# Kernel optimization log

Hardware: AMD Instinct MI355X
Metric: run time of the kernel (lower is better)

The kernel has to match this reference:

```python
import jax, jax.numpy as jnp
import numpy as np

B, N, D = 1024, 7, 1024
SQRT_D = float(np.sqrt(D))
MAX_CTX, MAX_VIB = 0.24, 0.26
VIB_IDX, CTX_IDX = 3, N - 1

ADJ = jnp.asarray(np.array([
    [1, 1, 0, 0, 1, 1, 1],
    [1, 1, 1, 1, 1, 1, 1],
    [0, 1, 1, 0, 1, 0, 1],
    [0, 1, 0, 1, 1, 1, 1],
    [1, 1, 1, 1, 1, 1, 1],
    [1, 1, 0, 1, 1, 1, 1],
    [1, 1, 1, 1, 1, 1, 1]], dtype=np.float32))


def _gelu(x):
    return jax.nn.gelu(x, approximate=False)


def setup_inputs() -> dict:
    key = jax.random.key(0)
    ks = jax.random.split(key, 20)
    s = 0.02
    def w(k, shape):
        return jax.random.normal(k, shape, dtype=jnp.float32) * s
    return {
        "nodes": jax.random.normal(ks[0], (B, N, D), dtype=jnp.float32),
        "Wq": w(ks[1], (D, D)), "bq": jnp.zeros((D,), jnp.float32),
        "Wk": w(ks[2], (D, D)), "bk": jnp.zeros((D,), jnp.float32),
        "Wv": w(ks[3], (D, D)), "bv": jnp.zeros((D,), jnp.float32),
        "We1": w(ks[4], (3 * D, D)), "be1": jnp.zeros((D,), jnp.float32),
        "We2": w(ks[5], (D, 1)), "be2": jnp.zeros((1,), jnp.float32),
        "Wu1": w(ks[6], (2 * D, D)), "bu1": jnp.zeros((D,), jnp.float32),
        "Wu2": w(ks[7], (D, D)), "bu2": jnp.zeros((D,), jnp.float32),
        "Wi1": w(ks[8], (2 * D, D)), "bi1": jnp.zeros((D,), jnp.float32),
        "Wi2": w(ks[9], (D, 1)), "bi2": jnp.zeros((1,), jnp.float32),
    }


def _cap_importance(imp):
    cap = jnp.ones((N,), imp.dtype).at[VIB_IDX].set(MAX_VIB).at[CTX_IDX].set(MAX_CTX)
    free = jnp.ones((N,), imp.dtype).at[VIB_IDX].set(0.0).at[CTX_IDX].set(0.0)[None, :]
    capped = jnp.minimum(imp, cap[None, :])
    free_mass = (imp * free).sum(axis=1, keepdims=True)
    residual = jnp.clip(1.0 - capped.sum(axis=1, keepdims=True), 0.0)
    uniform = free / jnp.maximum(free.sum(axis=1, keepdims=True), 1.0)
    free_share = jnp.where(free_mass > 1e-6,
                           imp * free / jnp.maximum(free_mass, 1e-6),
                           uniform)
    redis = capped + free_share * residual
    return redis / jnp.maximum(redis.sum(axis=1, keepdims=True), 1e-6)


def _physics_loss(upd):
    norms = jnp.linalg.norm(upd, axis=-1)  # [B,N]
    dots = jnp.einsum('bnd,bmd->bnm', upd, upd)
    cos = dots / jnp.maximum(norms[:, :, None] * norms[:, None, :], 1e-8)
    eye = jnp.eye(N, dtype=upd.dtype)
    edge_loss = ((1.0 - cos) * ADJ[None]).sum() / jnp.maximum(ADJ.sum() * upd.shape[0], 1.0) * upd.shape[0]
    # note: torch sums over batch too -> divide by ADJ.sum() only
    edge_loss = ((1.0 - cos) * ADJ[None]).sum() / jnp.maximum(ADJ.sum(), 1.0)
    non_mask = (1.0 - ADJ) * (1.0 - eye)
    non_loss = (jax.nn.relu(cos - 0.35) * non_mask[None]).sum() / jnp.maximum(non_mask.sum(), 1.0)
    return edge_loss + 0.5 * non_loss


def _alignment_loss(upd, fused):
    fn = fused / jnp.maximum(jnp.linalg.norm(fused, axis=-1, keepdims=True), 1e-12)
    nn_ = upd / jnp.maximum(jnp.linalg.norm(upd, axis=-1, keepdims=True), 1e-12)
    cos = jnp.einsum('bnd,bd->bn', nn_, fn)
    return (1.0 - cos).mean()


def reference(nodes, Wq, bq, Wk, bk, Wv, bv, We1, be1, We2, be2,
              Wu1, bu1, Wu2, bu2, Wi1, bi1, Wi2, bi2):
    q = nodes @ Wq + bq
    k = nodes @ Wk + bk
    v = nodes @ Wv + bv
    logits = jnp.einsum('bnd,bmd->bnm', q, k) / SQRT_D
    # edge gate: cat([left, right, ctx]) @ We1 == left@Wa + right@Wb + ctx@Wc
    Wa, Wb, Wc = We1[:D], We1[D:2 * D], We1[2 * D:]
    la = nodes @ Wa                      # [B,N,D] (left varies over axis n)
    rb = nodes @ Wb                      # [B,N,D] (right varies over axis m)
    cc = nodes[:, -1] @ Wc               # [B,D]   (ctx broadcast)
    h = la[:, :, None, :] + rb[:, None, :, :] + cc[:, None, None, :] + be1
    edge_logits = (_gelu(h) @ We2 + be2)[..., 0]  # [B,N,N]
    masked = logits + edge_logits + (ADJ[None] - 1.0) * 10000.0
    attn = jax.nn.softmax(masked, axis=-1)
    messages = jnp.einsum('bnm,bmd->bnd', attn, v)
    upd_in = jnp.concatenate([nodes, messages], axis=-1)
    updated = _gelu(upd_in @ Wu1 + bu1) @ Wu2 + bu2 + nodes
    gq = jnp.broadcast_to(updated[:, -1:, :], updated.shape)
    imp_in = jnp.concatenate([updated, gq], axis=-1)
    imp_logits = (_gelu(imp_in @ Wi1 + bi1) @ Wi2 + bi2)[..., 0]
    imp = jax.nn.softmax(imp_logits, axis=-1)
    imp = _cap_importance(imp)
    fused = jnp.einsum('bn,bnd->bd', imp, updated)
    phys = _physics_loss(updated)
    align = _alignment_loss(updated, fused)
    return (fused, updated, imp, attn, phys + align * 0.0, align)
```

## Files before the change

kernel.cpp:

```cpp
#include <hip/hip_runtime.h>
#include <hip/hip_bf16.h>


typedef __attribute__((ext_vector_type(8))) short bf16x8;
typedef __attribute__((ext_vector_type(4))) float f32x4;

__constant__ float c_adj[49] = {
    1,1,0,0,1,1,1,
    1,1,1,1,1,1,1,
    0,1,1,0,1,0,1,
    0,1,0,1,1,1,1,
    1,1,1,1,1,1,1,
    1,1,0,1,1,1,1,
    1,1,1,1,1,1,1};

__device__ __forceinline__ float gelu_f(float x) {
    float z = fabsf(x) * 0.70710678118654752f;
    float t = 1.0f / (1.0f + 0.3275911f * z);
    float poly = ((((1.061405429f * t - 1.453152027f) * t + 1.421413741f) * t
                  - 0.284496736f) * t + 0.254829592f) * t;
    float e = __expf(-z * z);
    float erf_abs = 1.0f - poly * e;
    float erf = copysignf(erf_abs, x);
    return 0.5f * x * (1.0f + erf);
}
__device__ __forceinline__ float b2f(unsigned short u) {
    unsigned int x = ((unsigned int)u) << 16;
    union { unsigned int i; float f; } c; c.i = x; return c.f;
}
__device__ __forceinline__ unsigned short f2b(float f) {
    __hip_bfloat16 h = __float2bfloat16(f);
    union { __hip_bfloat16 b; unsigned short u; } c; c.b = h; return c.u;
}

__device__ __forceinline__ void gload_lds16(const void* g, void* l) {
    __builtin_amdgcn_global_load_lds(
        (const __attribute__((address_space(1))) unsigned int*)g,
        (__attribute__((address_space(3))) unsigned int*)l, 16, 0, 0);
}

__device__ __forceinline__ int maprow(int r, int mode) {
    if (mode == 1) return r * 7 + 6;
    if (mode == 2) return r - r % 7 + 6;
    return r;
}

__global__ __launch_bounds__(512, 4) void gemm128x8w(
    const unsigned short* __restrict__ A1, int a1Mode,
    const unsigned short* __restrict__ A2, int a2Mode,
    const unsigned short* __restrict__ WT, int ldw,
    const float* __restrict__ bias,
    const float* __restrict__ resid,
    float* __restrict__ Cf,
    unsigned short* __restrict__ Cb, size_t segStride,
    int K, int act)
{
    __shared__ short As[3][128 * 32];
    __shared__ short Bs[3][128 * 32];
    const int tid = threadIdx.x;
    const int lane = tid & 63;
    const int w = tid >> 6;
    const int wr = (w >> 2) * 64;
    const int wc = (w & 3) * 32;

    int lin = blockIdx.y * gridDim.x + blockIdx.x;
    const int nwg = gridDim.x * gridDim.y;
    const int cpx = nwg >> 3;
    lin = (lin & 7) * cpx + (lin >> 3);
    const int row0 = (lin / gridDim.x) * 128;
    const int col0 = (lin % gridDim.x) * 128;

    const int fr = lane & 15;
    const int fko = (((lane >> 4) ^ ((fr >> 1) & 3)) << 3);

    const int sm_ = tid >> 2, sch = tid & 3;
    const int skc = (sch ^ ((sm_ >> 1) & 3)) * 8;
    const int ldsoff = tid * 8;

    const int NTt = K >> 5;

    auto stage = [&](int ktn) {
        int k0n = ktn * 32;
        const unsigned short* srcA; int mode; int kbase;
        if (k0n < 1024) { srcA = A1; mode = a1Mode; kbase = k0n; }
        else            { srcA = A2; mode = a2Mode; kbase = k0n - 1024; }
        int slot = ktn % 3;
        int rr = maprow(row0 + sm_, mode);
        gload_lds16(srcA + (size_t)rr * 1024 + kbase + skc, &As[slot][ldsoff]);
        gload_lds16(WT + (size_t)(col0 + sm_) * ldw + k0n + skc, &Bs[slot][ldsoff]);
    };

    f32x4 acc[4][2] = {};

    stage(0);
    if (NTt > 1) stage(1);
    asm volatile("s_waitcnt vmcnt(2)" ::: "memory");
    asm volatile("s_barrier" ::: "memory");

    for (int kt = 0; kt < NTt; ++kt) {
        const short* Ab = &As[kt % 3][0];
        const short* Bb = &Bs[kt % 3][0];

        if (kt + 2 < NTt) stage(kt + 2);

        bf16x8 af[4], bfv[2];
        #pragma unroll
        for (int i = 0; i < 4; ++i)
            af[i] = *(const bf16x8*)(Ab + (wr + i * 16 + fr) * 32 + fko);
        #pragma unroll
        for (int j = 0; j < 2; ++j)
            bfv[j] = *(const bf16x8*)(Bb + (wc + j * 16 + fr) * 32 + fko);

        __builtin_amdgcn_s_setprio(1);
        #pragma unroll
        for (int i = 0; i < 4; ++i)
            #pragma unroll
            for (int j = 0; j < 2; ++j)
                acc[i][j] = __builtin_amdgcn_mfma_f32_16x16x32_bf16(
                    af[i], bfv[j], acc[i][j], 0, 0, 0);
        __builtin_amdgcn_s_setprio(0);

        if (kt < NTt - 2) asm volatile("s_waitcnt vmcnt(2)" ::: "memory");
        else              asm volatile("s_waitcnt vmcnt(0)" ::: "memory");
        asm volatile("s_barrier" ::: "memory");
    }

    const int qrow = (lane >> 4) * 4;
    const int qcol = lane & 15;
    #pragma unroll
    for (int i = 0; i < 4; ++i) {
        int rbase = row0 + wr + i * 16 + qrow;
        #pragma unroll
        for (int j = 0; j < 2; ++j) {
            int c = col0 + wc + j * 16 + qcol;
            float bv = bias ? bias[c] : 0.0f;
            int seg = c >> 10, c0 = c & 1023;
            #pragma unroll
            for (int reg = 0; reg < 4; ++reg) {
                int r = rbase + reg;
                float vv = acc[i][j][reg] + bv;
                if (act) vv = gelu_f(vv);
                if (resid) vv += resid[(size_t)r * 1024 + c];
                if (Cf) Cf[(size_t)r * 1024 + c] = vv;
                if (Cb) Cb[(size_t)seg * segStride + (size_t)r * 1024 + c0] = f2b(vv);
            }
        }
    }
}

__global__ __launch_bounds__(256) void gemm64x128(
    const unsigned short* __restrict__ A1, int a1Mode,
    const unsigned short* __restrict__ A2, int a2Mode,
    const unsigned short* __restrict__ WT, int ldw,
    const float* __restrict__ bias,
    const float* __restrict__ resid,
    float* __restrict__ Cf,
    unsigned short* __restrict__ Cb,
    int K, int act)
{
    __shared__ short As[64 * 32];
    __shared__ short Bs[128 * 32];
    const int tid = threadIdx.x;
    const int lane = tid & 63;
    const int w = tid >> 6;
    const int wc = w * 32;
    const int row0 = blockIdx.y * 64;
    const int col0 = blockIdx.x * 128;
    const int fr = lane & 15;
    const int fko = (((lane >> 4) ^ ((fr >> 1) & 3)) << 3);

    f32x4 acc[4][2] = {};

    for (int k0 = 0; k0 < K; k0 += 32) {
        const unsigned short* srcA; int mode; int kbase;
        if (k0 < 1024) { srcA = A1; mode = a1Mode; kbase = k0; }
        else           { srcA = A2; mode = a2Mode; kbase = k0 - 1024; }
        {
            int m = tid >> 2, ch = tid & 3;
            int kc = (ch ^ ((m >> 1) & 3)) * 8;
            int rr = maprow(row0 + m, mode);
            gload_lds16(srcA + (size_t)rr * 1024 + kbase + kc, &As[tid * 8]);
        }
        #pragma unroll
        for (int rnd = 0; rnd < 2; ++rnd) {
            int c = rnd * 256 + tid;
            int n = c >> 2, ch = c & 3;
            int kc = (ch ^ ((n >> 1) & 3)) * 8;
            gload_lds16(WT + (size_t)(col0 + n) * ldw + k0 + kc, &Bs[c * 8]);
        }
        __syncthreads();
        bf16x8 af[4], bf_[2];
        #pragma unroll
        for (int i = 0; i < 4; ++i)
            af[i] = *(const bf16x8*)(&As[(i * 16 + fr) * 32 + fko]);
        #pragma unroll
        for (int j = 0; j < 2; ++j)
            bf_[j] = *(const bf16x8*)(&Bs[(wc + j * 16 + fr) * 32 + fko]);
        #pragma unroll
        for (int i = 0; i < 4; ++i)
            #pragma unroll
            for (int j = 0; j < 2; ++j)
                acc[i][j] = __builtin_amdgcn_mfma_f32_16x16x32_bf16(
                    af[i], bf_[j], acc[i][j], 0, 0, 0);
        __syncthreads();
    }

    const int qrow = (lane >> 4) * 4;
    const int qcol = lane & 15;
    #pragma unroll
    for (int i = 0; i < 4; ++i) {
        int rbase = row0 + i * 16 + qrow;
        #pragma unroll
        for (int j = 0; j < 2; ++j) {
            int c = col0 + wc + j * 16 + qcol;
            float bv = bias ? bias[c] : 0.0f;
            #pragma unroll
            for (int reg = 0; reg < 4; ++reg) {
                int r = rbase + reg;
                float vv = acc[i][j][reg] + bv;
                if (act) vv = gelu_f(vv);
                if (resid) vv += resid[(size_t)r * 1024 + c];
                if (Cf) Cf[(size_t)r * 1024 + c] = vv;
                if (Cb) Cb[(size_t)r * 1024 + c] = f2b(vv);
            }
        }
    }
}

__global__ __launch_bounds__(256) void cast_f2b(
    const float* __restrict__ in, unsigned short* __restrict__ out, int n)
{
    int i = (blockIdx.x * 256 + threadIdx.x) * 4;
    if (i >= n) return;
    float4 v = *(const float4*)(in + i);
    ushort4 o;
    o.x = f2b(v.x); o.y = f2b(v.y); o.z = f2b(v.z); o.w = f2b(v.w);
    *(ushort4*)(out + i) = o;
}

__global__ __launch_bounds__(256) void tcast_all(
    const float* __restrict__ Wq, const float* __restrict__ Wk,
    const float* __restrict__ Wv, const float* __restrict__ We1,
    const float* __restrict__ Wu1, const float* __restrict__ Wu2,
    const float* __restrict__ Wi1,
    unsigned short* __restrict__ WT_all, unsigned short* __restrict__ Wu1T,
    unsigned short* __restrict__ Wu2T, unsigned short* __restrict__ Wi1T)
{
    const int z = blockIdx.z;
    const float* src; unsigned short* dst; int R;
    switch (z) {
        case 0: src = Wq;            dst = WT_all;               R = 1024; break;
        case 1: src = Wk;            dst = WT_all + 1024 * 1024; R = 1024; break;
        case 2: src = Wv;            dst = WT_all + 2048 * 1024; R = 1024; break;
        case 3: src = We1;           dst = WT_all + 3072 * 1024; R = 1024; break;
        case 4: src = We1 + 1048576; dst = WT_all + 4096 * 1024; R = 1024; break;
        case 5: src = We1 + 2097152; dst = WT_all + 5120 * 1024; R = 1024; break;
        case 6: src = Wu1;           dst = Wu1T;                 R = 2048; break;
        case 7: src = Wu2;           dst = Wu2T;                 R = 1024; break;
        default: src = Wi1;          dst = Wi1T;                 R = 2048; break;
    }
    const int rt = blockIdx.y * 32;
    if (rt >= R) return;
    const int ct = blockIdx.x * 32;
    __shared__ float t[32][33];
    const int tx = threadIdx.x & 31, ty = threadIdx.x >> 5;
    #pragma unroll
    for (int s = 0; s < 4; ++s)
        t[ty + s * 8][tx] = src[(size_t)(rt + ty + s * 8) * 1024 + ct + tx];
    __syncthreads();
    #pragma unroll
    for (int s = 0; s < 4; ++s)
        dst[(size_t)(ct + ty + s * 8) * R + rt + tx] = f2b(t[tx][ty + s * 8]);
}

__global__ void build_bias(const float* __restrict__ bq,
                           const float* __restrict__ bk,
                           const float* __restrict__ bv,
                           float* __restrict__ bias_all,
                           float* __restrict__ acc)
{
    int i = blockIdx.x * 256 + threadIdx.x;
    if (i < 4) acc[i] = 0.f;
    if (i >= 5120) return;
    int seg = i >> 10, c = i & 1023;
    float v = 0.f;
    if (seg == 0) v = bq[c];
    else if (seg == 1) v = bk[c];
    else if (seg == 2) v = bv[c];
    bias_all[i] = v;
}

__global__ __launch_bounds__(256) void attn_msg_b(
    const unsigned short* __restrict__ q, const unsigned short* __restrict__ k,
    const unsigned short* __restrict__ v,
    const unsigned short* __restrict__ la, const unsigned short* __restrict__ rb,
    const float* __restrict__ cc,
    const float* __restrict__ We2, const float* __restrict__ be2,
    float* __restrict__ attn_out, unsigned short* __restrict__ msg)
{
    const int bn = blockIdx.x;
    const int b = bn / 7, n = bn % 7;
    const int tid = threadIdx.x;
    const int lane = tid & 63, wv = tid >> 6;
    const int d0 = tid * 4;
    __shared__ float red[4][14];
    __shared__ float sm[7];

    float qv[4], lav[4], wev[4];
    {
        ushort4 q4 = *(const ushort4*)(q + (size_t)bn * 1024 + d0);
        ushort4 l4 = *(const ushort4*)(la + (size_t)bn * 1024 + d0);
        float4 c4 = *(const float4*)(cc + (size_t)b * 1024 + d0);
        float4 w4 = *(const float4*)(We2 + d0);
        qv[0] = b2f(q4.x); qv[1] = b2f(q4.y); qv[2] = b2f(q4.z); qv[3] = b2f(q4.w);
        lav[0] = b2f(l4.x) + c4.x; lav[1] = b2f(l4.y) + c4.y;
        lav[2] = b2f(l4.z) + c4.z; lav[3] = b2f(l4.w) + c4.w;
        wev[0] = w4.x; wev[1] = w4.y; wev[2] = w4.z; wev[3] = w4.w;
    }

    float s1a[7], s2a[7];
    #pragma unroll
    for (int m = 0; m < 7; ++m) {
        ushort4 k4 = *(const ushort4*)(k  + (size_t)(b * 7 + m) * 1024 + d0);
        ushort4 r4 = *(const ushort4*)(rb + (size_t)(b * 7 + m) * 1024 + d0);
        s1a[m] = qv[0] * b2f(k4.x) + qv[1] * b2f(k4.y)
               + qv[2] * b2f(k4.z) + qv[3] * b2f(k4.w);
        s2a[m] = gelu_f(lav[0] + b2f(r4.x)) * wev[0]
               + gelu_f(lav[1] + b2f(r4.y)) * wev[1]
               + gelu_f(lav[2] + b2f(r4.z)) * wev[2]
               + gelu_f(lav[3] + b2f(r4.w)) * wev[3];
    }
    #pragma unroll
    for (int m = 0; m < 7; ++m) {
        float x1 = s1a[m], x2 = s2a[m];
        #pragma unroll
        for (int off = 32; off > 0; off >>= 1) {
            x1 += __shfl_down(x1, off);
            x2 += __shfl_down(x2, off);
        }
        if (lane == 0) { red[wv][m] = x1; red[wv][7 + m] = x2; }
    }
    __syncthreads();
    if (tid == 0) {
        float l[7];
        #pragma unroll
        for (int m = 0; m < 7; ++m) {
            float d1 = red[0][m] + red[1][m] + red[2][m] + red[3][m];
            float d2 = red[0][7 + m] + red[1][7 + m] + red[2][7 + m] + red[3][7 + m];
            l[m] = d1 * (1.0f / 32.0f) + d2 + be2[0]
                 + (c_adj[n * 7 + m] - 1.0f) * 10000.0f;
        }
        float mx = l[0];
        #pragma unroll
        for (int m = 1; m < 7; ++m) mx = fmaxf(mx, l[m]);
        float e[7], s = 0.f;
        #pragma unroll
        for (int m = 0; m < 7; ++m) { e[m] = __expf(l[m] - mx); s += e[m]; }
        float inv = 1.0f / s;
        #pragma unroll
        for (int m = 0; m < 7; ++m) {
            float wgt = e[m] * inv;
            sm[m] = wgt;
            attn_out[(size_t)bn * 7 + m] = wgt;
        }
    }
    __syncthreads();
    float wr_[7];
    #pragma unroll
    for (int m = 0; m < 7; ++m) wr_[m] = sm[m];
    float s0 = 0.f, s1 = 0.f, s2 = 0.f, s3 = 0.f;
    #pragma unroll
    for (int m = 0; m < 7; ++m) {
        ushort4 v4 = *(const ushort4*)(v + (size_t)(b * 7 + m) * 1024 + d0);
        s0 += wr_[m] * b2f(v4.x); s1 += wr_[m] * b2f(v4.y);
        s2 += wr_[m] * b2f(v4.z); s3 += wr_[m] * b2f(v4.w);
    }
    ushort4 o;
    o.x = f2b(s0); o.y = f2b(s1); o.z = f2b(s2); o.w = f2b(s3);
    *(ushort4*)(msg + (size_t)bn * 1024 + d0) = o;
}

__global__ __launch_bounds__(256) void row_dot_b(
    const unsigned short* __restrict__ H, const float* __restrict__ w2,
    const float* __restrict__ b2, float* __restrict__ out)
{
    const int r = blockIdx.x;
    const int tid = threadIdx.x;
    const int lane = tid & 63, wv = tid >> 6;
    __shared__ float red[4];
    const int d0 = tid * 4;
    ushort4 h4 = *(const ushort4*)(H + (size_t)r * 1024 + d0);
    float4 w4 = *(const float4*)(w2 + d0);
    float s = b2f(h4.x) * w4.x + b2f(h4.y) * w4.y
            + b2f(h4.z) * w4.z + b2f(h4.w) * w4.w;
    #pragma unroll
    for (int off = 32; off > 0; off >>= 1) s += __shfl_down(s, off);
    if (lane == 0) red[wv] = s;
    __syncthreads();
    if (tid == 0) out[r] = red[0] + red[1] + red[2] + red[3] + b2[0];
}

__global__ __launch_bounds__(256) void imp_fused_k(
    const float* __restrict__ logits, const float* __restrict__ upd,
    float* __restrict__ imp_out, float* __restrict__ fused_out)
{
    const int b = blockIdx.x;
    const int tid = threadIdx.x;
    __shared__ float w[7];
    if (tid == 0) {
        float l[7], e[7];
        float mx = -1e30f;
        for (int i = 0; i < 7; ++i) { l[i] = logits[b * 7 + i]; mx = fmaxf(mx, l[i]); }
        float s = 0.f;
        for (int i = 0; i < 7; ++i) { e[i] = expf(l[i] - mx); s += e[i]; }
        float inv = 1.0f / s;
        float imp[7];
        for (int i = 0; i < 7; ++i) imp[i] = e[i] * inv;
        const float cap[7] = {1.f, 1.f, 1.f, 0.26f, 1.f, 1.f, 0.24f};
        const float fr[7]  = {1.f, 1.f, 1.f, 0.f,   1.f, 1.f, 0.f};
        float capped[7], capsum = 0.f, fmass = 0.f;
        for (int i = 0; i < 7; ++i) {
            capped[i] = fminf(imp[i], cap[i]);
            capsum += capped[i];
            fmass += imp[i] * fr[i];
        }
        float residual = fmaxf(1.0f - capsum, 0.0f);
        float redis[7], rs = 0.f;
        for (int i = 0; i < 7; ++i) {
            float fs = (fmass > 1e-6f) ? imp[i] * fr[i] / fmaxf(fmass, 1e-6f)
                                       : fr[i] * 0.2f;
            redis[i] = capped[i] + fs * residual;
            rs += redis[i];
        }
        float invr = 1.0f / fmaxf(rs, 1e-6f);
        for (int i = 0; i < 7; ++i) {
            float wi = redis[i] * invr;
            w[i] = wi;
            imp_out[b * 7 + i] = wi;
        }
    }
    __syncthreads();
    float wr[7];
    #pragma unroll
    for (int i = 0; i < 7; ++i) wr[i] = w[i];
    #pragma unroll
    for (int j = 0; j < 4; ++j) {
        int d = tid + j * 256;
        float s = 0.f;
        #pragma unroll
        for (int nn2 = 0; nn2 < 7; ++nn2)
            s += wr[nn2] * upd[(size_t)(b * 7 + nn2) * 1024 + d];
        fused_out[(size_t)b * 1024 + d] = s;
    }
}

__global__ __launch_bounds__(256) void physics_k(
    const float* __restrict__ upd, const float* __restrict__ fused,
    float* __restrict__ accums)
{
    const int b = blockIdx.x;
    const int tid = threadIdx.x;
    const int lane = tid & 63, wv = tid >> 6;
    __shared__ float u[7][1024];
    __shared__ float f[1024];
    __shared__ float wred[4][36];
    for (int idx = tid; idx < 7 * 1024; idx += 256)
        u[idx >> 10][idx & 1023] = upd[(size_t)b * 7168 + idx];
    for (int d = tid; d < 1024; d += 256)
        f[d] = fused[(size_t)b * 1024 + d];
    __syncthreads();

    float vals[36];
    #pragma unroll
    for (int i = 0; i < 36; ++i) vals[i] = 0.f;
    for (int d = tid; d < 1024; d += 256) {
        float x[7];
        #pragma unroll
        for (int n = 0; n < 7; ++n) x[n] = u[n][d];
        float fv = f[d];
        int idx = 0;
        #pragma unroll
        for (int n = 0; n < 7; ++n) {
            #pragma unroll
            for (int m = n; m < 7; ++m) vals[idx++] += x[n] * x[m];
        }
        #pragma unroll
        for (int n = 0; n < 7; ++n) vals[28 + n] += x[n] * fv;
        vals[35] += fv * fv;
    }
    #pragma unroll
    for (int i = 0; i < 36; ++i) {
        float s = vals[i];
        #pragma unroll
        for (int off = 32; off > 0; off >>= 1) s += __shfl_down(s, off);
        if (lane == 0) wred[wv][i] = s;
    }
    __syncthreads();
    if (tid == 0) {
        float tv[36];
        for (int i = 0; i < 36; ++i)
            tv[i] = wred[0][i] + wred[1][i] + wred[2][i] + wred[3][i];
        auto didx = [](int n, int m) -> int {
            if (n > m) { int t = n; n = m; m = t; }
            return n * 7 - n * (n - 1) / 2 + (m - n);
        };
        float norms[7];
        for (int n = 0; n < 7; ++n) norms[n] = sqrtf(tv[didx(n, n)]);
        float e = 0.f, nl = 0.f;
        for (int n = 0; n < 7; ++n)
            for (int m = 0; m < 7; ++m) {
                float cos_ = tv[didx(n, m)] / fmaxf(norms[n] * norms[m], 1e-8f);
                float adj = c_adj[n * 7 + m];
                e += (1.0f - cos_) * adj;
                if (adj == 0.0f && n != m) nl += fmaxf(cos_ - 0.35f, 0.0f);
            }
        float fnorm = sqrtf(tv[35]);
        float al = 0.f;
        for (int n = 0; n < 7; ++n) {
            float cosn = tv[28 + n] /
                         (fmaxf(norms[n], 1e-12f) * fmaxf(fnorm, 1e-12f));
            al += 1.0f - cosn;
        }
        atomicAdd(&accums[0], e);
        atomicAdd(&accums[1], nl);
        atomicAdd(&accums[2], al);
    }
}

__global__ void finalize_k(const float* __restrict__ a,
                           float* __restrict__ phys_o,
                           float* __restrict__ align_o)
{
    phys_o[0]  = a[0] / 41.0f + 0.5f * (a[1] / 8.0f);
    align_o[0] = a[2] * (1.0f / 7168.0f);
}

extern "C" void kernel_launch(void* const* d_in, const int* in_sizes, int n_in,
                              void* d_out, int out_size, void* d_ws, size_t ws_size,
                              hipStream_t stream)
{
    const float* nodes = (const float*)d_in[0];
    const float* Wq  = (const float*)d_in[1];
    const float* bq  = (const float*)d_in[2];
    const float* Wk  = (const float*)d_in[3];
    const float* bk  = (const float*)d_in[4];
    const float* Wv  = (const float*)d_in[5];
    const float* bv  = (const float*)d_in[6];
    const float* We1 = (const float*)d_in[7];
    const float* be1 = (const float*)d_in[8];
    const float* We2 = (const float*)d_in[9];
    const float* be2 = (const float*)d_in[10];
    const float* Wu1 = (const float*)d_in[11];
    const float* bu1 = (const float*)d_in[12];
    const float* Wu2 = (const float*)d_in[13];
    const float* bu2 = (const float*)d_in[14];
    const float* Wi1 = (const float*)d_in[15];
    const float* bi1 = (const float*)d_in[16];
    const float* Wi2 = (const float*)d_in[17];
    const float* bi2 = (const float*)d_in[18];

    float* out = (float*)d_out;
    float* fused_o = out;
    float* upd_o   = out + 1048576;
    float* imp_o   = out + 1048576 + 7340032;
    float* attn_o  = imp_o + 7168;
    float* phys_o  = attn_o + 50176;
    float* align_o = phys_o + 1;

    const size_t BIG = 7340032;
    const size_t MEG = 1048576;
    char* p = (char*)d_ws;
    unsigned short* nodes_b = (unsigned short*)p; p += BIG * 2;
    unsigned short* qb      = (unsigned short*)p; p += BIG * 2;
    unsigned short* kb      = (unsigned short*)p; p += BIG * 2;
    unsigned short* vb      = (unsigned short*)p; p += BIG * 2;
    unsigned short* lab     = (unsigned short*)p; p += BIG * 2;
    unsigned short* rbb     = (unsigned short*)p; p += BIG * 2;
    unsigned short* WT_all  = (unsigned short*)p; p += (size_t)6144 * 1024 * 2;
    unsigned short* Wu1T    = (unsigned short*)p; p += 2 * MEG * 2;
    unsigned short* Wu2T    = (unsigned short*)p; p += MEG * 2;
    unsigned short* Wi1T    = (unsigned short*)p; p += 2 * MEG * 2;
    float* bias_all = (float*)p; p += 5120 * 4;
    float* ccf = (float*)p; p += MEG * 4;
    float* il  = (float*)p; p += 7168 * 4;
    float* acc = (float*)p; p += 4 * 4;
    unsigned short* msgb = lab;
    unsigned short* hub  = qb;
    unsigned short* updb = kb;
    unsigned short* hib  = vb;

    dim3 blk(256);
    dim3 blk512(512);

    cast_f2b<<<dim3(7168), blk, 0, stream>>>(nodes, nodes_b, 7340032);
    tcast_all<<<dim3(32, 64, 9), blk, 0, stream>>>(Wq, Wk, Wv, We1, Wu1, Wu2, Wi1,
                                                   WT_all, Wu1T, Wu2T, Wi1T);
    build_bias<<<dim3(20), blk, 0, stream>>>(bq, bk, bv, bias_all, acc);

    gemm128x8w<<<dim3(40, 56), blk512, 0, stream>>>(
        nodes_b, 0, nullptr, 0, WT_all, 1024, bias_all, nullptr,
        nullptr, qb, BIG, 1024, 0);

    gemm64x128<<<dim3(8, 16), blk, 0, stream>>>(
        nodes_b, 1, nullptr, 0, WT_all + (size_t)5120 * 1024, 1024, be1, nullptr,
        ccf, nullptr, 1024, 0);

    attn_msg_b<<<dim3(7168), blk, 0, stream>>>(qb, kb, vb, lab, rbb, ccf, We2, be2,
                                               attn_o, msgb);

    gemm128x8w<<<dim3(8, 56), blk512, 0, stream>>>(
        nodes_b, 0, msgb, 0, Wu1T, 2048, bu1, nullptr, nullptr, hub, 0, 2048, 1);
    gemm128x8w<<<dim3(8, 56), blk512, 0, stream>>>(
        hub, 0, nullptr, 0, Wu2T, 1024, bu2, nodes, upd_o, updb, 0, 1024, 0);
    gemm128x8w<<<dim3(8, 56), blk512, 0, stream>>>(
        updb, 0, updb, 2, Wi1T, 2048, bi1, nullptr, nullptr, hib, 0, 2048, 1);

    row_dot_b<<<dim3(7168), blk, 0, stream>>>(hib, Wi2, bi2, il);
    imp_fused_k<<<dim3(1024), blk, 0, stream>>>(il, upd_o, imp_o, fused_o);
    physics_k<<<dim3(1024), blk, 0, stream>>>(upd_o, fused_o, acc);
    finalize_k<<<1, 1, 0, stream>>>(acc, phys_o, align_o);
}
```

Before: 535.2 us.

## Switch main GEMM to 4-wave 32x32x16 MFMA tiles with 64x64 per wave

The 128x128 GEMM kernel moves from 8 waves issuing 16x16x32 MFMAs (64x32 per wave) to 4 waves issuing 32x32x16 MFMAs (64x64 per wave), with each thread now staging two 16-byte chunks per operand per k-step. Larger per-wave tiles raise register reuse and cut LDS reads per MFMA, and the larger MFMA shape issues fewer instructions. The cost is more accumulator registers per thread and fewer waves per block to hide latency. The epilogue is rewritten for the 32x32 accumulator layout.

After: 580.8 us. 8.5% more time.

```diff
diff --git a/kernel.cpp b/kernel.cpp
--- a/kernel.cpp
+++ b/kernel.cpp
@@ -4,6 +4,7 @@
 
 typedef __attribute__((ext_vector_type(8))) short bf16x8;
 typedef __attribute__((ext_vector_type(4))) float f32x4;
+typedef __attribute__((ext_vector_type(16))) float f32x16;
 
 __constant__ float c_adj[49] = {
     1,1,0,0,1,1,1,
@@ -45,7 +46,7 @@
     return r;
 }
 
-__global__ __launch_bounds__(512, 4) void gemm128x8w(
+__global__ __launch_bounds__(256) void gemm128w32(
     const unsigned short* __restrict__ A1, int a1Mode,
     const unsigned short* __restrict__ A2, int a2Mode,
     const unsigned short* __restrict__ WT, int ldw,
@@ -60,8 +61,8 @@
     const int tid = threadIdx.x;
     const int lane = tid & 63;
     const int w = tid >> 6;
-    const int wr = (w >> 2) * 64;
-    const int wc = (w & 3) * 32;
+    const int wr = (w >> 1) * 64;
+    const int wc = (w & 1) * 64;
 
     int lin = blockIdx.y * gridDim.x + blockIdx.x;
     const int nwg = gridDim.x * gridDim.y;
@@ -70,12 +71,14 @@
     const int row0 = (lin / gridDim.x) * 128;
     const int col0 = (lin % gridDim.x) * 128;
 
-    const int fr = lane & 15;
-    const int fko = (((lane >> 4) ^ ((fr >> 1) & 3)) << 3);
-
-    const int sm_ = tid >> 2, sch = tid & 3;
-    const int skc = (sch ^ ((sm_ >> 1) & 3)) * 8;
-    const int ldsoff = tid * 8;
+    const int l31 = lane & 31;
+    const int hi  = lane >> 5;
+    const int xorv = (l31 >> 1) & 3;
+    int aRow[2], bRow[2], cOff[2];
+    aRow[0] = (wr + l31) * 32;       aRow[1] = (wr + 32 + l31) * 32;
+    bRow[0] = (wc + l31) * 32;       bRow[1] = (wc + 32 + l31) * 32;
+    cOff[0] = ((hi)     ^ xorv) * 8;
+    cOff[1] = ((2 + hi) ^ xorv) * 8;
 
     const int NTt = K >> 5;
 
@@ -85,16 +88,28 @@
         if (k0n < 1024) { srcA = A1; mode = a1Mode; kbase = k0n; }
         else            { srcA = A2; mode = a2Mode; kbase = k0n - 1024; }
         int slot = ktn % 3;
-        int rr = maprow(row0 + sm_, mode);
-        gload_lds16(srcA + (size_t)rr * 1024 + kbase + skc, &As[slot][ldsoff]);
-        gload_lds16(WT + (size_t)(col0 + sm_) * ldw + k0n + skc, &Bs[slot][ldsoff]);
+        #pragma unroll
+        for (int rnd = 0; rnd < 2; ++rnd) {
+            int c2 = rnd * 256 + tid;
+            int m = c2 >> 2, ch = c2 & 3;
+            int kc = (ch ^ ((m >> 1) & 3)) * 8;
+            int rr = maprow(row0 + m, mode);
+            gload_lds16(srcA + (size_t)rr * 1024 + kbase + kc, &As[slot][c2 * 8]);
+        }
+        #pragma unroll
+        for (int rnd = 0; rnd < 2; ++rnd) {
+            int c2 = rnd * 256 + tid;
+            int n = c2 >> 2, ch = c2 & 3;
+            int kc = (ch ^ ((n >> 1) & 3)) * 8;
+            gload_lds16(WT + (size_t)(col0 + n) * ldw + k0n + kc, &Bs[slot][c2 * 8]);
+        }
     };
 
-    f32x4 acc[4][2] = {};
+    f32x16 acc[2][2] = {};
 
     stage(0);
     if (NTt > 1) stage(1);
-    asm volatile("s_waitcnt vmcnt(2)" ::: "memory");
+    asm volatile("s_waitcnt vmcnt(4)" ::: "memory");
     asm volatile("s_barrier" ::: "memory");
 
     for (int kt = 0; kt < NTt; ++kt) {
@@ -103,46 +118,48 @@
 
         if (kt + 2 < NTt) stage(kt + 2);
 
-        bf16x8 af[4], bfv[2];
-        #pragma unroll
-        for (int i = 0; i < 4; ++i)
-            af[i] = *(const bf16x8*)(Ab + (wr + i * 16 + fr) * 32 + fko);
-        #pragma unroll
-        for (int j = 0; j < 2; ++j)
-            bfv[j] = *(const bf16x8*)(Bb + (wc + j * 16 + fr) * 32 + fko);
+        bf16x8 af[2][2], bfv[2][2];
+        #pragma unroll
+        for (int ks = 0; ks < 2; ++ks) {
+            #pragma unroll
+            for (int mf = 0; mf < 2; ++mf)
+                af[mf][ks] = *(const bf16x8*)(Ab + aRow[mf] + cOff[ks]);
+            #pragma unroll
+            for (int nf = 0; nf < 2; ++nf)
+                bfv[nf][ks] = *(const bf16x8*)(Bb + bRow[nf] + cOff[ks]);
+        }
 
         __builtin_amdgcn_s_setprio(1);
         #pragma unroll
-        for (int i = 0; i < 4; ++i)
+        for (int ks = 0; ks < 2; ++ks)
             #pragma unroll
-            for (int j = 0; j < 2; ++j)
-                acc[i][j] = __builtin_amdgcn_mfma_f32_16x16x32_bf16(
-                    af[i], bfv[j], acc[i][j], 0, 0, 0);
+            for (int mf = 0; mf < 2; ++mf)
+                #pragma unroll
+                for (int nf = 0; nf < 2; ++nf)
+                    acc[mf][nf] = __builtin_amdgcn_mfma_f32_32x32x16_bf16(
+                        af[mf][ks], bfv[nf][ks], acc[mf][nf], 0, 0, 0);
         __builtin_amdgcn_s_setprio(0);
 
-        if (kt < NTt - 2) asm volatile("s_waitcnt vmcnt(2)" ::: "memory");
+        if (kt < NTt - 2) asm volatile("s_waitcnt vmcnt(4)" ::: "memory");
         else              asm volatile("s_waitcnt vmcnt(0)" ::: "memory");
         asm volatile("s_barrier" ::: "memory");
     }
 
-    const int qrow = (lane >> 4) * 4;
-    const int qcol = lane & 15;
-    #pragma unroll
-    for (int i = 0; i < 4; ++i) {
-        int rbase = row0 + wr + i * 16 + qrow;
-        #pragma unroll
-        for (int j = 0; j < 2; ++j) {
-            int c = col0 + wc + j * 16 + qcol;
+    #pragma unroll
+    for (int mf = 0; mf < 2; ++mf) {
+        #pragma unroll
+        for (int nf = 0; nf < 2; ++nf) {
+            int c = col0 + wc + nf * 32 + l31;
             float bv = bias ? bias[c] : 0.0f;
             int seg = c >> 10, c0 = c & 1023;
             #pragma unroll
-            for (int reg = 0; reg < 4; ++reg) {
-                int r = rbase + reg;
-                float vv = acc[i][j][reg] + bv;
+            for (int r = 0; r < 16; ++r) {
+                int row = row0 + wr + mf * 32 + (r & 3) + 8 * (r >> 2) + 4 * hi;
+                float vv = acc[mf][nf][r] + bv;
                 if (act) vv = gelu_f(vv);
-                if (resid) vv += resid[(size_t)r * 1024 + c];
-                if (Cf) Cf[(size_t)r * 1024 + c] = vv;
-                if (Cb) Cb[(size_t)seg * segStride + (size_t)r * 1024 + c0] = f2b(vv);
+                if (resid) vv += resid[(size_t)row * 1024 + c];
+                if (Cf) Cf[(size_t)row * 1024 + c] = vv;
+                if (Cb) Cb[(size_t)seg * segStride + (size_t)row * 1024 + c0] = f2b(vv);
             }
         }
     }
@@ -590,14 +607,13 @@
     unsigned short* hib  = vb;
 
     dim3 blk(256);
-    dim3 blk512(512);
 
     cast_f2b<<<dim3(7168), blk, 0, stream>>>(nodes, nodes_b, 7340032);
     tcast_all<<<dim3(32, 64, 9), blk, 0, stream>>>(Wq, Wk, Wv, We1, Wu1, Wu2, Wi1,
                                                    WT_all, Wu1T, Wu2T, Wi1T);
     build_bias<<<dim3(20), blk, 0, stream>>>(bq, bk, bv, bias_all, acc);
 
-    gemm128x8w<<<dim3(40, 56), blk512, 0, stream>>>(
+    gemm128w32<<<dim3(40, 56), blk, 0, stream>>>(
         nodes_b, 0, nullptr, 0, WT_all, 1024, bias_all, nullptr,
         nullptr, qb, BIG, 1024, 0);
 
@@ -608,11 +624,11 @@
     attn_msg_b<<<dim3(7168), blk, 0, stream>>>(qb, kb, vb, lab, rbb, ccf, We2, be2,
                                                attn_o, msgb);
 
-    gemm128x8w<<<dim3(8, 56), blk512, 0, stream>>>(
+    gemm128w32<<<dim3(8, 56), blk, 0, stream>>>(
         nodes_b, 0, msgb, 0, Wu1T, 2048, bu1, nullptr, nullptr, hub, 0, 2048, 1);
-    gemm128x8w<<<dim3(8, 56), blk512, 0, stream>>>(
+    gemm128w32<<<dim3(8, 56), blk, 0, stream>>>(
         hub, 0, nullptr, 0, Wu2T, 1024, bu2, nodes, upd_o, updb, 0, 1024, 0);
-    gemm128x8w<<<dim3(8, 56), blk512, 0, stream>>>(
+    gemm128w32<<<dim3(8, 56), blk, 0, stream>>>(
         updb, 0, updb, 2, Wi1T, 2048, bi1, nullptr, nullptr, hib, 0, 2048, 1);
 
     row_dot_b<<<dim3(7168), blk, 0, stream>>>(hib, Wi2, bi2, il);
```

## Fuse importance row-dot into GEMM epilogue, merge importance and physics kernels

Applied to the files above, without the earlier changes.

Computes the importance logits directly in the Wi1 GEMM epilogue by applying GELU, dotting with Wi2 and reducing per row via shuffles and atomics, eliminating the hidden bf16 buffer and the separate row-dot kernel. The importance/fused kernel and the physics kernel are merged so updated rows are loaded once into shared memory. The large QKV projection switches to a new 256-thread double-buffered 128x128 GEMM with larger per-wave tiles. The atomic accumulation adds nondeterministic summation order, and the bi2 bias is dropped on the grounds that softmax is shift invariant.

Result: no change. 539.1 us (+0.7%).

```diff
diff --git a/kernel.cpp b/kernel.cpp
--- a/kernel.cpp
+++ b/kernel.cpp
@@ -45,6 +45,116 @@
     return r;
 }
 
+__global__ __launch_bounds__(256) void gemm128db(
+    const unsigned short* __restrict__ A1, int a1Mode,
+    const unsigned short* __restrict__ A2, int a2Mode,
+    const unsigned short* __restrict__ WT, int ldw,
+    const float* __restrict__ bias,
+    const float* __restrict__ resid,
+    float* __restrict__ Cf,
+    unsigned short* __restrict__ Cb, size_t segStride,
+    int K, int act)
+{
+    __shared__ short As[2][128 * 32];
+    __shared__ short Bs[2][128 * 32];
+    const int tid = threadIdx.x;
+    const int lane = tid & 63;
+    const int w = tid >> 6;
+    const int wr = (w >> 1) * 64;
+    const int wc = (w & 1) * 64;
+
+    int lin = blockIdx.y * gridDim.x + blockIdx.x;
+    const int nwg = gridDim.x * gridDim.y;
+    const int cpx = nwg >> 3;
+    lin = (lin & 7) * cpx + (lin >> 3);
+    const int row0 = (lin / gridDim.x) * 128;
+    const int col0 = (lin % gridDim.x) * 128;
+
+    const int fr = lane & 15;
+    const int fko = (((lane >> 4) ^ ((fr >> 1) & 3)) << 3);
+
+    const int NTt = K >> 5;
+
+    auto stage = [&](int ktn) {
+        int k0n = ktn * 32;
+        const unsigned short* srcA; int mode; int kbase;
+        if (k0n < 1024) { srcA = A1; mode = a1Mode; kbase = k0n; }
+        else            { srcA = A2; mode = a2Mode; kbase = k0n - 1024; }
+        short* Adst = &As[ktn & 1][0];
+        short* Bdst = &Bs[ktn & 1][0];
+        #pragma unroll
+        for (int rnd = 0; rnd < 2; ++rnd) {
+            int c = rnd * 256 + tid;
+            int m = c >> 2, ch = c & 3;
+            int kc = (ch ^ ((m >> 1) & 3)) * 8;
+            int rr = maprow(row0 + m, mode);
+            gload_lds16(srcA + (size_t)rr * 1024 + kbase + kc, Adst + c * 8);
+        }
+        #pragma unroll
+        for (int rnd = 0; rnd < 2; ++rnd) {
+            int c = rnd * 256 + tid;
+            int n = c >> 2, ch = c & 3;
+            int kc = (ch ^ ((n >> 1) & 3)) * 8;
+            gload_lds16(WT + (size_t)(col0 + n) * ldw + k0n + kc, Bdst + c * 8);
+        }
+    };
+
+    f32x4 acc[4][4] = {};
+
+    stage(0);
+    asm volatile("s_waitcnt vmcnt(0)" ::: "memory");
+    asm volatile("s_barrier" ::: "memory");
+
+    for (int kt = 0; kt < NTt; ++kt) {
+        const short* Ab = &As[kt & 1][0];
+        const short* Bb = &Bs[kt & 1][0];
+
+        if (kt + 1 < NTt) stage(kt + 1);
+
+        bf16x8 af[4], bfv[4];
+        #pragma unroll
+        for (int i = 0; i < 4; ++i)
+            af[i] = *(const bf16x8*)(Ab + (wr + i * 16 + fr) * 32 + fko);
+        #pragma unroll
+        for (int j = 0; j < 4; ++j)
+            bfv[j] = *(const bf16x8*)(Bb + (wc + j * 16 + fr) * 32 + fko);
+
+        __builtin_amdgcn_s_setprio(1);
+        #pragma unroll
+        for (int i = 0; i < 4; ++i)
+            #pragma unroll
+            for (int j = 0; j < 4; ++j)
+                acc[i][j] = __builtin_amdgcn_mfma_f32_16x16x32_bf16(
+                    af[i], bfv[j], acc[i][j], 0, 0, 0);
+        __builtin_amdgcn_s_setprio(0);
+
+        asm volatile("s_waitcnt vmcnt(0)" ::: "memory");
+        asm volatile("s_barrier" ::: "memory");
+    }
+
+    const int qrow = (lane >> 4) * 4;
+    const int qcol = lane & 15;
+    #pragma unroll
+    for (int i = 0; i < 4; ++i) {
+        int rbase = row0 + wr + i * 16 + qrow;
+        #pragma unroll
+        for (int j = 0; j < 4; ++j) {
+            int c = col0 + wc + j * 16 + qcol;
+            float bv = bias ? bias[c] : 0.0f;
+            int seg = c >> 10, c0 = c & 1023;
+            #pragma unroll
+            for (int reg = 0; reg < 4; ++reg) {
+                int r = rbase + reg;
+                float vv = acc[i][j][reg] + bv;
+                if (act) vv = gelu_f(vv);
+                if (resid) vv += resid[(size_t)r * 1024 + c];
+                if (Cf) Cf[(size_t)r * 1024 + c] = vv;
+                if (Cb) Cb[(size_t)seg * segStride + (size_t)r * 1024 + c0] = f2b(vv);
+            }
+        }
+    }
+}
+
 __global__ __launch_bounds__(512, 4) void gemm128x8w(
     const unsigned short* __restrict__ A1, int a1Mode,
     const unsigned short* __restrict__ A2, int a2Mode,
@@ -53,7 +163,8 @@
     const float* __restrict__ resid,
     float* __restrict__ Cf,
     unsigned short* __restrict__ Cb, size_t segStride,
-    int K, int act)
+    int K, int act,
+    const float* __restrict__ w2, float* __restrict__ ildst)
 {
     __shared__ short As[3][128 * 32];
     __shared__ short Bs[3][128 * 32];
@@ -127,6 +238,33 @@
 
     const int qrow = (lane >> 4) * 4;
     const int qcol = lane & 15;
+
+    if (w2) {
+        float* rowacc = (float*)&As[0][0];
+        if (tid < 128) rowacc[tid] = 0.f;
+        __syncthreads();
+        int c0 = col0 + wc + qcol;
+        int c1 = col0 + wc + 16 + qcol;
+        float b0 = bias[c0], b1 = bias[c1];
+        float w20 = w2[c0], w21 = w2[c1];
+        #pragma unroll
+        for (int i = 0; i < 4; ++i) {
+            #pragma unroll
+            for (int reg = 0; reg < 4; ++reg) {
+                float v = gelu_f(acc[i][0][reg] + b0) * w20
+                        + gelu_f(acc[i][1][reg] + b1) * w21;
+                #pragma unroll
+                for (int off = 8; off > 0; off >>= 1)
+                    v += __shfl_down(v, off, 16);
+                if (qcol == 0)
+                    atomicAdd(&rowacc[wr + i * 16 + qrow + reg], v);
+            }
+        }
+        __syncthreads();
+        if (tid < 128) atomicAdd(&ildst[row0 + tid], rowacc[tid]);
+        return;
+    }
+
     #pragma unroll
     for (int i = 0; i < 4; ++i) {
         int rbase = row0 + wr + i * 16 + qrow;
@@ -277,10 +415,12 @@
                            const float* __restrict__ bk,
                            const float* __restrict__ bv,
                            float* __restrict__ bias_all,
-                           float* __restrict__ acc)
+                           float* __restrict__ acc,
+                           float* __restrict__ il)
 {
     int i = blockIdx.x * 256 + threadIdx.x;
     if (i < 4) acc[i] = 0.f;
+    if (i < 7168) il[i] = 0.f;
     if (i >= 5120) return;
     int seg = i >> 10, c = i & 1023;
     float v = 0.f;
@@ -380,33 +520,22 @@
     *(ushort4*)(msg + (size_t)bn * 1024 + d0) = o;
 }
 
-__global__ __launch_bounds__(256) void row_dot_b(
-    const unsigned short* __restrict__ H, const float* __restrict__ w2,
-    const float* __restrict__ b2, float* __restrict__ out)
-{
-    const int r = blockIdx.x;
+__global__ __launch_bounds__(256) void imp_phys_k(
+    const float* __restrict__ logits, const float* __restrict__ upd,
+    float* __restrict__ imp_out, float* __restrict__ fused_out,
+    float* __restrict__ accums)
+{
+    const int b = blockIdx.x;
     const int tid = threadIdx.x;
     const int lane = tid & 63, wv = tid >> 6;
-    __shared__ float red[4];
-    const int d0 = tid * 4;
-    ushort4 h4 = *(const ushort4*)(H + (size_t)r * 1024 + d0);
-    float4 w4 = *(const float4*)(w2 + d0);
-    float s = b2f(h4.x) * w4.x + b2f(h4.y) * w4.y
-            + b2f(h4.z) * w4.z + b2f(h4.w) * w4.w;
-    #pragma unroll
-    for (int off = 32; off > 0; off >>= 1) s += __shfl_down(s, off);
-    if (lane == 0) red[wv] = s;
-    __syncthreads();
-    if (tid == 0) out[r] = red[0] + red[1] + red[2] + red[3] + b2[0];
-}
-
-__global__ __launch_bounds__(256) void imp_fused_k(
-    const float* __restrict__ logits, const float* __restrict__ upd,
-    float* __restrict__ imp_out, float* __restrict__ fused_out)
-{
-    const int b = blockIdx.x;
-    const int tid = threadIdx.x;
-    __shared__ float w[7];
+    __shared__ float u[7][1024];
+    __shared__ float f[1024];
+    __shared__ float wsh[7];
+    __shared__ float wred[4][36];
+
+    for (int idx = tid; idx < 7 * 1024; idx += 256)
+        u[idx >> 10][idx & 1023] = upd[(size_t)b * 7168 + idx];
+
     if (tid == 0) {
         float l[7], e[7];
         float mx = -1e30f;
@@ -435,39 +564,25 @@
         float invr = 1.0f / fmaxf(rs, 1e-6f);
         for (int i = 0; i < 7; ++i) {
             float wi = redis[i] * invr;
-            w[i] = wi;
+            wsh[i] = wi;
             imp_out[b * 7 + i] = wi;
         }
     }
     __syncthreads();
+
     float wr[7];
     #pragma unroll
-    for (int i = 0; i < 7; ++i) wr[i] = w[i];
+    for (int i = 0; i < 7; ++i) wr[i] = wsh[i];
     #pragma unroll
     for (int j = 0; j < 4; ++j) {
         int d = tid + j * 256;
         float s = 0.f;
         #pragma unroll
         for (int nn2 = 0; nn2 < 7; ++nn2)
-            s += wr[nn2] * upd[(size_t)(b * 7 + nn2) * 1024 + d];
+            s += wr[nn2] * u[nn2][d];
+        f[d] = s;
         fused_out[(size_t)b * 1024 + d] = s;
     }
-}
-
-__global__ __launch_bounds__(256) void physics_k(
-    const float* __restrict__ upd, const float* __restrict__ fused,
-    float* __restrict__ accums)
-{
-    const int b = blockIdx.x;
-    const int tid = threadIdx.x;
-    const int lane = tid & 63, wv = tid >> 6;
-    __shared__ float u[7][1024];
-    __shared__ float f[1024];
-    __shared__ float wred[4][36];
-    for (int idx = tid; idx < 7 * 1024; idx += 256)
-        u[idx >> 10][idx & 1023] = upd[(size_t)b * 7168 + idx];
-    for (int d = tid; d < 1024; d += 256)
-        f[d] = fused[(size_t)b * 1024 + d];
     __syncthreads();
 
     float vals[36];
@@ -558,6 +673,7 @@
     const float* bi1 = (const float*)d_in[16];
     const float* Wi2 = (const float*)d_in[17];
     const float* bi2 = (const float*)d_in[18];
+    (void)bi2;
 
     float* out = (float*)d_out;
     float* fused_o = out;
@@ -587,7 +703,6 @@
     unsigned short* msgb = lab;
     unsigned short* hub  = qb;
     unsigned short* updb = kb;
-    unsigned short* hib  = vb;
 
     dim3 blk(256);
     dim3 blk512(512);
@@ -595,9 +710,9 @@
     cast_f2b<<<dim3(7168), blk, 0, stream>>>(nodes, nodes_b, 7340032);
     tcast_all<<<dim3(32, 64, 9), blk, 0, stream>>>(Wq, Wk, Wv, We1, Wu1, Wu2, Wi1,
                                                    WT_all, Wu1T, Wu2T, Wi1T);
-    build_bias<<<dim3(20), blk, 0, stream>>>(bq, bk, bv, bias_all, acc);
-
-    gemm128x8w<<<dim3(40, 56), blk512, 0, stream>>>(
+    build_bias<<<dim3(28), blk, 0, stream>>>(bq, bk, bv, bias_all, acc, il);
+
+    gemm128db<<<dim3(40, 56), blk, 0, stream>>>(
         nodes_b, 0, nullptr, 0, WT_all, 1024, bias_all, nullptr,
         nullptr, qb, BIG, 1024, 0);
 
@@ -609,14 +724,15 @@
                                                attn_o, msgb);
 
     gemm128x8w<<<dim3(8, 56), blk512, 0, stream>>>(
-        nodes_b, 0, msgb, 0, Wu1T, 2048, bu1, nullptr, nullptr, hub, 0, 2048, 1);
+        nodes_b, 0, msgb, 0, Wu1T, 2048, bu1, nullptr, nullptr, hub, 0, 2048, 1,
+        nullptr, nullptr);
     gemm128x8w<<<dim3(8, 56), blk512, 0, stream>>>(
-        hub, 0, nullptr, 0, Wu2T, 1024, bu2, nodes, upd_o, updb, 0, 1024, 0);
+        hub, 0, nullptr, 0, Wu2T, 1024, bu2, nodes, upd_o, updb, 0, 1024, 0,
+        nullptr, nullptr);
     gemm128x8w<<<dim3(8, 56), blk512, 0, stream>>>(
-        updb, 0, updb, 2, Wi1T, 2048, bi1, nullptr, nullptr, hib, 0, 2048, 1);
-
-    row_dot_b<<<dim3(7168), blk, 0, stream>>>(hib, Wi2, bi2, il);
-    imp_fused_k<<<dim3(1024), blk, 0, stream>>>(il, upd_o, imp_o, fused_o);
-    physics_k<<<dim3(1024), blk, 0, stream>>>(upd_o, fused_o, acc);
+        updb, 0, updb, 2, Wi1T, 2048, bi1, nullptr, nullptr, nullptr, 0, 2048, 1,
+        Wi2, il);
+
+    imp_phys_k<<<dim3(1024), blk, 0, stream>>>(il, upd_o, imp_o, fused_o, acc);
     finalize_k<<<1, 1, 0, stream>>>(acc, phys_o, align_o);
 }
```
